# Kernel optimization log

Measured on AMD Instinct MI355X. Metric: run time of the kernel, lower is better.

The kernel has to match this reference:

```python
import jax, jax.numpy as jnp
import numpy as np

B, L, H = 32, 2048, 512


def setup_inputs() -> dict:
    key = jax.random.key(0)
    k1, k2, k3, k4, k5, k6 = jax.random.split(key, 6)
    scale = 1.0 / np.sqrt(H)
    return {
        "query": jax.random.normal(k1, (B, H), dtype=jnp.float32),
        "ref": jax.random.normal(k2, (B, L, H), dtype=jnp.float32),
        "mask": jax.random.randint(k3, (B, L), 0, 2) == 1,
        # learned params (torch Linear weight layout: [out, in]; apply as x @ W.T)
        "W_ref": jax.random.normal(k4, (H, H), dtype=jnp.float32) * scale,
        "W_q": jax.random.normal(k5, (H, H), dtype=jnp.float32) * scale,
        "v": jax.random.normal(k6, (H,), dtype=jnp.float32) * scale,
    }


def reference(query, ref, mask, W_ref, W_q, v):
    scale = 1.0 / np.sqrt(H)
    # additive (Bahdanau) scores: v^T tanh(W_ref ref + W_q q)
    encoded_ref = jnp.einsum("blh,oh->blo", ref, W_ref)          # (B, L, H)
    encoded_q = jnp.einsum("bh,oh->bo", query, W_q)[:, None, :]  # (B, 1, H)
    scores = jnp.einsum("blh,h->bl", jnp.tanh(encoded_ref + encoded_q), v)
    scores = scores * scale
    scores = jnp.where(mask, -1e9, scores)
    attn = jax.nn.softmax(scores, axis=1)                         # (B, L)
    glimpse = jnp.einsum("bl,blh->bh", attn, ref)                 # (B, H)
    return glimpse, scores
```

## Files before the change

kernel.cpp:

```cpp
#include <hip/hip_runtime.h>
#include <hip/hip_bf16.h>
#include <cstdint>

typedef __attribute__((ext_vector_type(4))) float f32x4;
typedef __attribute__((ext_vector_type(8))) short s16x8;

#define NB   32
#define NL   2048
#define NH   512
#define NM   (NB * NL)
#define SCALE 0.04419417382415922f

__device__ __forceinline__ ushort f2bf(float f) {
    __hip_bfloat16 b = __float2bfloat16(f);
    return *reinterpret_cast<ushort*>(&b);
}
__device__ __forceinline__ unsigned long long pack4(float4 f) {
    union { ushort u[4]; unsigned long long v; } p;
    p.u[0] = f2bf(f.x); p.u[1] = f2bf(f.y); p.u[2] = f2bf(f.z); p.u[3] = f2bf(f.w);
    return p.v;
}

#define GL16(g, l)                                                         \
    __builtin_amdgcn_global_load_lds(                                      \
        (const __attribute__((address_space(1))) unsigned int*)(g),        \
        (__attribute__((address_space(3))) unsigned int*)(l), 16, 0, 0)

__global__ __launch_bounds__(256) void k_pre(const float* __restrict__ W,
                                             ushort* __restrict__ Wb,
                                             const float* __restrict__ query,
                                             const float* __restrict__ Wq,
                                             float* __restrict__ eq) {
    int bid = blockIdx.x;
    int t = threadIdx.x;
    if (bid < 64) {
        const float4* F = (const float4*)W;
        unsigned long long* U = (unsigned long long*)Wb;
        int base = bid * 1024 + t;
        float4 f[4];
#pragma unroll
        for (int k = 0; k < 4; ++k) f[k] = F[base + k * 256];
#pragma unroll
        for (int k = 0; k < 4; ++k) U[base + k * 256] = pack4(f[k]);
    } else {
        __shared__ float q[NH];
        int b = bid - 64;
        q[t] = query[b * NH + t];
        q[t + 256] = query[b * NH + t + 256];
        __syncthreads();
#pragma unroll
        for (int half = 0; half < 2; ++half) {
            int o = t + half * 256;
            const float4* w = (const float4*)(Wq + (size_t)o * NH);
            float acc = 0.f;
#pragma unroll 4
            for (int i = 0; i < NH / 4; ++i) {
                float4 x = w[i];
                acc += q[4 * i] * x.x + q[4 * i + 1] * x.y + q[4 * i + 2] * x.z + q[4 * i + 3] * x.w;
            }
            eq[b * NH + o] = acc;
        }
    }
}

__global__ __launch_bounds__(512, 4) void k_gemm_full(const float* __restrict__ ref,
                                                      const ushort* __restrict__ Wb,
                                                      const float* __restrict__ eq,
                                                      const float* __restrict__ v,
                                                      const int* __restrict__ mask,
                                                      float* __restrict__ out_sc) {
    __shared__ char smem[81920];
    ushort* Bs0 = (ushort*)smem;
    ushort* Bs1 = (ushort*)(smem + 32768);
    float*  As0 = (float*)(smem + 65536);
    float*  As1 = (float*)(smem + 73728);

    int tid = threadIdx.x;
    int lane = tid & 63, wid = tid >> 6;
    int blk = blockIdx.x;
    int m0g = blk << 6;
    int b = blk >> 5;

    f32x4 acc[4][4];
#pragma unroll
    for (int i = 0; i < 4; ++i)
#pragma unroll
        for (int j = 0; j < 4; ++j) acc[i][j] = (f32x4)(0.f);

    const ushort* bglob = Wb + ((size_t)(wid * 64) + (lane >> 2)) * NH + ((lane & 3) << 3);
    const float* aglob = ref + (size_t)(m0g + wid * 8 + (lane >> 3)) * NH
                             + (((lane & 7) ^ ((lane >> 3) & 7)) << 2);

    int lr = lane & 15, kq = lane >> 4;
    int bbase = (wid * 64 + lr) * 32 + (kq << 3);
    int arow = lr * 32;
    int ac0 = (((2 * kq) ^ (lr & 7)) << 2);
    int ac1 = (((2 * kq + 1) ^ (lr & 7)) << 2);

#define STAGE(Bsb, Asb, kt)                                           \
    {   GL16(bglob + (kt) * 32,            Bsb + (wid * 64) * 32);    \
        GL16(bglob + (kt) * 32 + 16 * NH,  Bsb + (wid * 64 + 16) * 32); \
        GL16(bglob + (kt) * 32 + 32 * NH,  Bsb + (wid * 64 + 32) * 32); \
        GL16(bglob + (kt) * 32 + 48 * NH,  Bsb + (wid * 64 + 48) * 32); \
        GL16(aglob + (kt) * 32,            Asb + (wid * 8) * 32); }

#define READ_CVT(Bsb, Asb)                                                       \
    _Pragma("unroll")                                                            \
    for (int f = 0; f < 4; ++f) bfr[f] = *(const s16x8*)&Bsb[bbase + f * 512];   \
    _Pragma("unroll")                                                            \
    for (int f = 0; f < 4; ++f) {                                                \
        float4 a0 = *(const float4*)(Asb + arow + f * 512 + ac0);                \
        float4 a1 = *(const float4*)(Asb + arow + f * 512 + ac1);                \
        union { ushort u[8]; s16x8 v; } p;                                       \
        p.u[0] = f2bf(a0.x); p.u[1] = f2bf(a0.y);                                \
        p.u[2] = f2bf(a0.z); p.u[3] = f2bf(a0.w);                                \
        p.u[4] = f2bf(a1.x); p.u[5] = f2bf(a1.y);                                \
        p.u[6] = f2bf(a1.z); p.u[7] = f2bf(a1.w);                                \
        af[f] = p.v;                                                             \
    }

#define MFMA_ALL()                                                               \
    __builtin_amdgcn_s_setprio(1);                                               \
    _Pragma("unroll")                                                            \
    for (int fr = 0; fr < 4; ++fr)                                               \
        _Pragma("unroll")                                                        \
        for (int fc = 0; fc < 4; ++fc)                                           \
            acc[fr][fc] = __builtin_amdgcn_mfma_f32_16x16x32_bf16(               \
                af[fr], bfr[fc], acc[fr][fc], 0, 0, 0);                          \
    __builtin_amdgcn_s_setprio(0);

    STAGE(Bs0, As0, 0)
    STAGE(Bs1, As1, 1)

#pragma unroll 1
    for (int t2 = 0; t2 < 7; ++t2) {
        {
            s16x8 bfr[4], af[4];
            asm volatile("s_waitcnt vmcnt(5)" ::: "memory");
            __builtin_amdgcn_s_barrier();
            READ_CVT(Bs0, As0)
            asm volatile("s_waitcnt lgkmcnt(0)" ::: "memory");
            __builtin_amdgcn_sched_barrier(0);
            __builtin_amdgcn_s_barrier();
            STAGE(Bs0, As0, 2 * t2 + 2)
            MFMA_ALL()
        }
        {
            s16x8 bfr[4], af[4];
            asm volatile("s_waitcnt vmcnt(5)" ::: "memory");
            __builtin_amdgcn_s_barrier();
            READ_CVT(Bs1, As1)
            asm volatile("s_waitcnt lgkmcnt(0)" ::: "memory");
            __builtin_amdgcn_sched_barrier(0);
            __builtin_amdgcn_s_barrier();
            STAGE(Bs1, As1, 2 * t2 + 3)
            MFMA_ALL()
        }
    }
    {
        s16x8 bfr[4], af[4];
        asm volatile("s_waitcnt vmcnt(5)" ::: "memory");
        __builtin_amdgcn_s_barrier();
        READ_CVT(Bs0, As0)
        MFMA_ALL()
    }
    {
        s16x8 bfr[4], af[4];
        asm volatile("s_waitcnt vmcnt(0)" ::: "memory");
        __builtin_amdgcn_s_barrier();
        READ_CVT(Bs1, As1)
        MFMA_ALL()
    }
#undef STAGE
#undef READ_CVT
#undef MFMA_ALL

    __syncthreads();

    float* sc_red = (float*)smem;
    const float* eqb = eq + b * NH;
    float vv[4], ee[4];
#pragma unroll
    for (int fc = 0; fc < 4; ++fc) {
        int c = wid * 64 + fc * 16 + lr;
        vv[fc] = v[c];
        ee[fc] = eqb[c];
    }
#pragma unroll
    for (int fr = 0; fr < 4; ++fr) {
#pragma unroll
        for (int reg = 0; reg < 4; ++reg) {
            float s = 0.f;
#pragma unroll
            for (int fc = 0; fc < 4; ++fc) {
                float x = acc[fr][fc][reg] + ee[fc];
                float t = 1.f - 2.f / (__expf(2.f * x) + 1.f);
                s += vv[fc] * t;
            }
            s += __shfl_xor(s, 1);
            s += __shfl_xor(s, 2);
            s += __shfl_xor(s, 4);
            s += __shfl_xor(s, 8);
            if (lr == 0) sc_red[wid * 64 + fr * 16 + kq * 4 + reg] = s;
        }
    }
    __syncthreads();
    if (tid < 64) {
        float t = 0.f;
#pragma unroll
        for (int w = 0; w < 8; ++w) t += sc_red[w * 64 + tid];
        t *= SCALE;
        int rg = m0g + tid;
        if (mask[rg] != 0) t = -1e9f;
        out_sc[rg] = t;
    }
}

__global__ __launch_bounds__(256) void k_smglp(const float* __restrict__ scores,
                                               const float* __restrict__ ref,
                                               float* __restrict__ glp) {
    int sp = blockIdx.x, b = blockIdx.y;
    int tid = threadIdx.x;
    int lane = tid & 63, wid = tid >> 6;
    __shared__ float red[4];
    __shared__ float asl[128];
    float sc[8];
    float mx = -3.4e38f;
#pragma unroll
    for (int i = 0; i < 8; ++i) {
        sc[i] = scores[b * NL + i * 256 + tid];
        mx = fmaxf(mx, sc[i]);
    }
#pragma unroll
    for (int o = 32; o >= 1; o >>= 1) mx = fmaxf(mx, __shfl_xor(mx, o));
    if (lane == 0) red[wid] = mx;
    __syncthreads();
    mx = fmaxf(fmaxf(red[0], red[1]), fmaxf(red[2], red[3]));
    __syncthreads();
    float ls = 0.f;
#pragma unroll
    for (int i = 0; i < 8; ++i) {
        float e = __expf(sc[i] - mx);
        ls += e;
        if (i == (sp >> 1) && (tid >> 7) == (sp & 1)) asl[tid & 127] = e;
    }
#pragma unroll
    for (int o = 32; o >= 1; o >>= 1) ls += __shfl_xor(ls, o);
    if (lane == 0) red[wid] = ls;
    __syncthreads();
    float inv = 1.f / (red[0] + red[1] + red[2] + red[3]);

    const float* rb = ref + ((size_t)b * NL + sp * 128) * NH;
    float2 acc = make_float2(0.f, 0.f);
#pragma unroll 4
    for (int l = 0; l < 128; ++l) {
        float a = asl[l];
        float2 r = ((const float2*)(rb + (size_t)l * NH))[tid];
        acc.x += a * r.x;
        acc.y += a * r.y;
    }
    acc.x *= inv;
    acc.y *= inv;
    ((float2*)(glp + (size_t)(sp * NB + b) * NH))[tid] = acc;
}

__global__ __launch_bounds__(256) void k_gred(const float* __restrict__ glp,
                                              float* __restrict__ out_gl) {
    int idx = blockIdx.x * 256 + threadIdx.x;
    float s = 0.f;
#pragma unroll
    for (int sp = 0; sp < 16; ++sp) s += glp[sp * (NB * NH) + idx];
    out_gl[idx] = s;
}

extern "C" void kernel_launch(void* const* d_in, const int* in_sizes, int n_in,
                              void* d_out, int out_size, void* d_ws, size_t ws_size,
                              hipStream_t stream) {
    const float* query = (const float*)d_in[0];
    const float* ref   = (const float*)d_in[1];
    const int*   mask  = (const int*)d_in[2];
    const float* W_ref = (const float*)d_in[3];
    const float* W_q   = (const float*)d_in[4];
    const float* v     = (const float*)d_in[5];

    float* out_gl = (float*)d_out;
    float* out_sc = out_gl + NB * NH;

    char* w = (char*)d_ws;
    ushort* wW = (ushort*)w;
    float* eq  = (float*)(w + 524288);
    float* glp = (float*)(w + 589824);

    k_pre<<<96, 256, 0, stream>>>(W_ref, wW, query, W_q, eq);
    k_gemm_full<<<1024, 512, 0, stream>>>(ref, wW, eq, v, mask, out_sc);
    k_smglp<<<dim3(16, NB), 256, 0, stream>>>(out_sc, ref, glp);
    k_gred<<<64, 256, 0, stream>>>(glp, out_gl);
}
```

Measured before the change: 120.7 us.

## Preload full A tile as bf16 in LDS once, stream only B

```diff
diff --git a/kernel.cpp b/kernel.cpp
--- a/kernel.cpp
+++ b/kernel.cpp
@@ -18,6 +18,12 @@
 __device__ __forceinline__ unsigned long long pack4(float4 f) {
     union { ushort u[4]; unsigned long long v; } p;
     p.u[0] = f2bf(f.x); p.u[1] = f2bf(f.y); p.u[2] = f2bf(f.z); p.u[3] = f2bf(f.w);
+    return p.v;
+}
+__device__ __forceinline__ s16x8 pack8(float4 a, float4 b) {
+    union { ushort u[8]; s16x8 v; } p;
+    p.u[0] = f2bf(a.x); p.u[1] = f2bf(a.y); p.u[2] = f2bf(a.z); p.u[3] = f2bf(a.w);
+    p.u[4] = f2bf(b.x); p.u[5] = f2bf(b.y); p.u[6] = f2bf(b.z); p.u[7] = f2bf(b.w);
     return p.v;
 }
 
@@ -63,17 +69,17 @@
     }
 }
 
-__global__ __launch_bounds__(512, 4) void k_gemm_full(const float* __restrict__ ref,
-                                                      const ushort* __restrict__ Wb,
-                                                      const float* __restrict__ eq,
-                                                      const float* __restrict__ v,
-                                                      const int* __restrict__ mask,
-                                                      float* __restrict__ out_sc) {
-    __shared__ char smem[81920];
+__global__ __launch_bounds__(512) void k_gemm_full(const float* __restrict__ ref,
+                                                   const ushort* __restrict__ Wb,
+                                                   const float* __restrict__ eq,
+                                                   const float* __restrict__ v,
+                                                   const int* __restrict__ mask,
+                                                   float* __restrict__ out_sc) {
+    __shared__ char smem[131072];
     ushort* Bs0 = (ushort*)smem;
     ushort* Bs1 = (ushort*)(smem + 32768);
-    float*  As0 = (float*)(smem + 65536);
-    float*  As1 = (float*)(smem + 73728);
+    ushort* As  = (ushort*)(smem + 65536);
+    float*  Atmp = (float*)smem;
 
     int tid = threadIdx.x;
     int lane = tid & 63, wid = tid >> 6;
@@ -81,43 +87,55 @@
     int m0g = blk << 6;
     int b = blk >> 5;
 
+#pragma unroll 1
+    for (int h = 0; h < 2; ++h) {
+        const float* ah = ref + (size_t)(m0g + h * 32) * NH;
+#pragma unroll
+        for (int i = 0; i < 8; ++i)
+            GL16(ah + (wid * 8 + i) * 256 + lane * 4,
+                 (ushort*)(smem + (wid * 8 + i) * 1024));
+        asm volatile("s_waitcnt vmcnt(0)" ::: "memory");
+        __syncthreads();
+        {
+            int r = tid >> 4, s = tid & 15;
+            const float4* src = (const float4*)(Atmp + r * 512 + s * 32);
+            float4 v0 = src[0], v1 = src[1], v2 = src[2], v3 = src[3];
+            float4 v4 = src[4], v5 = src[5], v6 = src[6], v7 = src[7];
+            int R = h * 32 + r;
+            ushort* dst = As + R * 512;
+            int rx = r & 7;
+            *(s16x8*)&dst[((s * 4 + 0) ^ rx) * 8] = pack8(v0, v1);
+            *(s16x8*)&dst[((s * 4 + 1) ^ rx) * 8] = pack8(v2, v3);
+            *(s16x8*)&dst[((s * 4 + 2) ^ rx) * 8] = pack8(v4, v5);
+            *(s16x8*)&dst[((s * 4 + 3) ^ rx) * 8] = pack8(v6, v7);
+        }
+        __syncthreads();
+    }
+
     f32x4 acc[4][4];
 #pragma unroll
     for (int i = 0; i < 4; ++i)
 #pragma unroll
         for (int j = 0; j < 4; ++j) acc[i][j] = (f32x4)(0.f);
 
+    int lr = lane & 15, kq = lane >> 4;
     const ushort* bglob = Wb + ((size_t)(wid * 64) + (lane >> 2)) * NH + ((lane & 3) << 3);
-    const float* aglob = ref + (size_t)(m0g + wid * 8 + (lane >> 3)) * NH
-                             + (((lane & 7) ^ ((lane >> 3) & 7)) << 2);
-
-    int lr = lane & 15, kq = lane >> 4;
     int bbase = (wid * 64 + lr) * 32 + (kq << 3);
-    int arow = lr * 32;
-    int ac0 = (((2 * kq) ^ (lr & 7)) << 2);
-    int ac1 = (((2 * kq + 1) ^ (lr & 7)) << 2);
-
-#define STAGE(Bsb, Asb, kt)                                           \
-    {   GL16(bglob + (kt) * 32,            Bsb + (wid * 64) * 32);    \
-        GL16(bglob + (kt) * 32 + 16 * NH,  Bsb + (wid * 64 + 16) * 32); \
-        GL16(bglob + (kt) * 32 + 32 * NH,  Bsb + (wid * 64 + 32) * 32); \
-        GL16(bglob + (kt) * 32 + 48 * NH,  Bsb + (wid * 64 + 48) * 32); \
-        GL16(aglob + (kt) * 32,            Asb + (wid * 8) * 32); }
-
-#define READ_CVT(Bsb, Asb)                                                       \
-    _Pragma("unroll")                                                            \
-    for (int f = 0; f < 4; ++f) bfr[f] = *(const s16x8*)&Bsb[bbase + f * 512];   \
-    _Pragma("unroll")                                                            \
-    for (int f = 0; f < 4; ++f) {                                                \
-        float4 a0 = *(const float4*)(Asb + arow + f * 512 + ac0);                \
-        float4 a1 = *(const float4*)(Asb + arow + f * 512 + ac1);                \
-        union { ushort u[8]; s16x8 v; } p;                                       \
-        p.u[0] = f2bf(a0.x); p.u[1] = f2bf(a0.y);                                \
-        p.u[2] = f2bf(a0.z); p.u[3] = f2bf(a0.w);                                \
-        p.u[4] = f2bf(a1.x); p.u[5] = f2bf(a1.y);                                \
-        p.u[6] = f2bf(a1.z); p.u[7] = f2bf(a1.w);                                \
-        af[f] = p.v;                                                             \
-    }
+    int lx7 = lr & 7;
+    int arow = lr * 512;
+
+#define STAGE_B(Bsb, kt)                                        \
+    {   _Pragma("unroll")                                       \
+        for (int j = 0; j < 4; ++j)                             \
+            GL16(bglob + (kt) * 32 + j * 16 * NH,               \
+                 (Bsb) + (wid * 64 + j * 16) * 32); }
+
+#define READ_FRAGS(Bsb, kt)                                                      \
+    {   int ac = (((kt) * 4 + kq) ^ lx7) << 3;                                   \
+        _Pragma("unroll")                                                        \
+        for (int f = 0; f < 4; ++f) af[f] = *(const s16x8*)&As[arow + f * 8192 + ac]; \
+        _Pragma("unroll")                                                        \
+        for (int f = 0; f < 4; ++f) bfr[f] = *(const s16x8*)&(Bsb)[bbase + f * 512]; }
 
 #define MFMA_ALL()                                                               \
     __builtin_amdgcn_s_setprio(1);                                               \
@@ -129,50 +147,48 @@
                 af[fr], bfr[fc], acc[fr][fc], 0, 0, 0);                          \
     __builtin_amdgcn_s_setprio(0);
 
-    STAGE(Bs0, As0, 0)
-    STAGE(Bs1, As1, 1)
+    STAGE_B(Bs0, 0)
+    STAGE_B(Bs1, 1)
 
 #pragma unroll 1
     for (int t2 = 0; t2 < 7; ++t2) {
-        {
-            s16x8 bfr[4], af[4];
-            asm volatile("s_waitcnt vmcnt(5)" ::: "memory");
+        {   s16x8 af[4], bfr[4];
+            asm volatile("s_waitcnt vmcnt(4)" ::: "memory");
             __builtin_amdgcn_s_barrier();
-            READ_CVT(Bs0, As0)
+            READ_FRAGS(Bs0, 2 * t2)
             asm volatile("s_waitcnt lgkmcnt(0)" ::: "memory");
             __builtin_amdgcn_sched_barrier(0);
             __builtin_amdgcn_s_barrier();
-            STAGE(Bs0, As0, 2 * t2 + 2)
+            STAGE_B(Bs0, 2 * t2 + 2)
             MFMA_ALL()
         }
-        {
-            s16x8 bfr[4], af[4];
-            asm volatile("s_waitcnt vmcnt(5)" ::: "memory");
+        {   s16x8 af[4], bfr[4];
+            asm volatile("s_waitcnt vmcnt(4)" ::: "memory");
             __builtin_amdgcn_s_barrier();
-            READ_CVT(Bs1, As1)
+            READ_FRAGS(Bs1, 2 * t2 + 1)
             asm volatile("s_waitcnt lgkmcnt(0)" ::: "memory");
             __builtin_amdgcn_sched_barrier(0);
             __builtin_amdgcn_s_barrier();
-            STAGE(Bs1, As1, 2 * t2 + 3)
+            STAGE_B(Bs1, 2 * t2 + 3)
             MFMA_ALL()
         }
     }
     {
-        s16x8 bfr[4], af[4];
-        asm volatile("s_waitcnt vmcnt(5)" ::: "memory");
+        s16x8 af[4], bfr[4];
+        asm volatile("s_waitcnt vmcnt(4)" ::: "memory");
         __builtin_amdgcn_s_barrier();
-        READ_CVT(Bs0, As0)
+        READ_FRAGS(Bs0, 14)
         MFMA_ALL()
     }
     {
-        s16x8 bfr[4], af[4];
+        s16x8 af[4], bfr[4];
         asm volatile("s_waitcnt vmcnt(0)" ::: "memory");
         __builtin_amdgcn_s_barrier();
-        READ_CVT(Bs1, As1)
+        READ_FRAGS(Bs1, 15)
         MFMA_ALL()
     }
-#undef STAGE
-#undef READ_CVT
+#undef STAGE_B
+#undef READ_FRAGS
 #undef MFMA_ALL
 
     __syncthreads();
```

After: 192.9 us. +59.9%, slower.
